# Kernel tuning notes

Hardware: AMD Instinct MI355X
Metric: run time of the kernel (lower is better)

## Reference

```python
import jax, jax.numpy as jnp
import numpy as np

N = 100000
E = 1600000
C = 128
SIM_THRESH = 0.2
DEG_THRESH = 3.0


def setup_inputs() -> dict:
    key = jax.random.key(0)
    ks = jax.random.split(key, 10)
    g = 0.1  # glorot-ish scale for prompt params
    x = jax.random.normal(ks[0], (N, C), jnp.float32)
    edge_index = jax.random.randint(ks[1], (2, E), 0, N)
    prompt_sim = jax.random.normal(ks[2], (1, C), jnp.float32) * g
    prompt_degree = jax.random.normal(ks[3], (1, C), jnp.float32) * g
    prompt_other = jax.random.normal(ks[4], (1, C), jnp.float32) * g
    readout_token = jax.random.normal(ks[5], (1, 1, C), jnp.float32) * g
    in_proj_w = jax.random.normal(ks[6], (3 * C, C), jnp.float32) / np.sqrt(C)
    in_proj_b = jnp.zeros((3 * C,), jnp.float32)
    out_proj_w = jax.random.normal(ks[7], (C, C), jnp.float32) / np.sqrt(C)
    out_proj_b = jnp.zeros((C,), jnp.float32)
    return {"x": x, "prompt_sim": prompt_sim, "prompt_degree": prompt_degree,
            "prompt_other": prompt_other, "readout_token": readout_token,
            "in_proj_w": in_proj_w, "in_proj_b": in_proj_b,
            "out_proj_w": out_proj_w, "out_proj_b": out_proj_b,
            "edge_index": edge_index}


def _forward(x, prompt_sim, prompt_degree, prompt_other, readout_token,
             in_proj_w, in_proj_b, out_proj_w, out_proj_b, edge_index):
    n = x.shape[0]
    row, col = edge_index[0], edge_index[1]

    # per-edge cosine similarity, scatter-added to destination nodes
    x_norm = x / jnp.sqrt(jnp.sum(x * x, axis=1, keepdims=True))  # [N,C]
    e = jnp.sum(x_norm[row] * x_norm[col], axis=1)                # [E]
    c = jax.ops.segment_sum(e, col, num_segments=n)               # [N]
    deg = jax.ops.segment_sum(jnp.ones_like(e), col, num_segments=n)  # [N]
    csim = jax.lax.stop_gradient(c / deg)                         # nan for deg==0 -> mask False

    sim_mask = csim <= SIM_THRESH                                 # [N] bool
    deg_mask = jax.lax.stop_gradient(deg) <= DEG_THRESH
    other_mask = ~(sim_mask | deg_mask)

    neg1 = jnp.float32(-1.0)
    slot0 = jnp.where(sim_mask[:, None], prompt_sim, neg1)        # [N,C]
    slot1 = jnp.where(deg_mask[:, None], prompt_degree, neg1)
    slot2 = jnp.where(other_mask[:, None], prompt_other, neg1)
    rec = jnp.stack([slot0, slot1, slot2], axis=1)                # [N,3,C]
    ro = jnp.broadcast_to(readout_token, (n, 1, x.shape[1]))
    rec = jnp.concatenate([ro, rec], axis=1)                      # [N,4,C]

    # key_padding_mask: True where slot entirely -1 (unfilled)
    kpm = jnp.all(rec == neg1, axis=-1)                           # [N,4]

    # single-head MHA over the 4 prompt slots per node
    qkv = rec @ in_proj_w.T + in_proj_b                           # [N,4,3C]
    q, k, v = jnp.split(qkv, 3, axis=-1)
    scale = 1.0 / np.sqrt(rec.shape[-1])
    scores = jnp.einsum('nqc,nkc->nqk', q, k) * scale             # [N,4,4]
    scores = jnp.where(kpm[:, None, :], -jnp.inf, scores)
    attn = jax.nn.softmax(scores, axis=-1)
    out = jnp.einsum('nqk,nkc->nqc', attn, v)
    out = out @ out_proj_w.T + out_proj_b                         # [N,4,C]

    final = out[:, 0, :]                                          # readout slot
    return x + final


def reference(x, prompt_sim, prompt_degree, prompt_other, readout_token,
              in_proj_w, in_proj_b, out_proj_w, out_proj_b, edge_index):
    return _forward(x, prompt_sim, prompt_degree, prompt_other, readout_token,
                    in_proj_w, in_proj_b, out_proj_w, out_proj_b, edge_index)
```

## Files before the change

### kernel.cpp

```cpp
#include <hip/hip_runtime.h>
#include <hip/hip_bf16.h>
#include <math.h>

#define C 128
#define SIM_THRESH 0.2f
#define DEG_THRESH 3.0f

#define FIX_SCALE 16777216.0f
#define FIX_INV   5.9604644775390625e-8f

typedef float floatx2 __attribute__((ext_vector_type(2)));

__device__ void finals_body(int combo,
                            const float* __restrict__ ps, const float* __restrict__ pd,
                            const float* __restrict__ po, const float* __restrict__ ro,
                            const float* __restrict__ W,  const float* __restrict__ b,
                            const float* __restrict__ Wo, const float* __restrict__ bo,
                            float* __restrict__ finals) {
    bool sim   = (combo & 1) != 0;
    bool degm  = (combo & 2) != 0;
    bool other = !(sim || degm);
    int t = threadIdx.x;

    __shared__ float rec[4][C];
    __shared__ float kk[4][C];
    __shared__ float vv[4][C];
    __shared__ float q0[C];
    __shared__ float out0[C];
    __shared__ float attn[4];

    if (t < C) {
        rec[0][t] = ro[t];
        rec[1][t] = sim   ? ps[t] : -1.0f;
        rec[2][t] = degm  ? pd[t] : -1.0f;
        rec[3][t] = other ? po[t] : -1.0f;
    }
    __syncthreads();

    if (t < C) {
        float accq = b[t];
        for (int i = 0; i < C; ++i) accq += rec[0][i] * W[t * C + i];
        q0[t] = accq;
        for (int j = 0; j < 4; ++j) {
            float ak = b[C + t];
            float av = b[2 * C + t];
            const float* Wk = W + (size_t)(C + t) * C;
            const float* Wv = W + (size_t)(2 * C + t) * C;
            for (int i = 0; i < C; ++i) {
                float r = rec[j][i];
                ak += r * Wk[i];
                av += r * Wv[i];
            }
            kk[j][t] = ak;
            vv[j][t] = av;
        }
    }
    __syncthreads();

    if (t == 0) {
        bool kpm[4] = { false, !sim, !degm, !other };
        const float scale = 0.08838834764831845f;
        float sc[4];
        float m = -INFINITY;
        for (int j = 0; j < 4; ++j) {
            if (kpm[j]) { sc[j] = -INFINITY; continue; }
            float s = 0.0f;
            for (int i = 0; i < C; ++i) s += q0[i] * kk[j][i];
            sc[j] = s * scale;
            m = fmaxf(m, sc[j]);
        }
        float denom = 0.0f;
        for (int j = 0; j < 4; ++j) {
            float e = (sc[j] == -INFINITY) ? 0.0f : expf(sc[j] - m);
            attn[j] = e;
            denom += e;
        }
        for (int j = 0; j < 4; ++j) attn[j] /= denom;
    }
    __syncthreads();

    if (t < C)
        out0[t] = attn[0] * vv[0][t] + attn[1] * vv[1][t] +
                  attn[2] * vv[2][t] + attn[3] * vv[3][t];
    __syncthreads();

    if (t < C) {
        float f = bo[t];
        for (int i = 0; i < C; ++i) f += out0[i] * Wo[t * C + i];
        finals[combo * C + t] = f;
    }
}

__global__ void prep_kernel(const float* __restrict__ x, unsigned int* __restrict__ xn,
                            unsigned long long* __restrict__ packed,
                            const float* __restrict__ ps, const float* __restrict__ pd,
                            const float* __restrict__ po, const float* __restrict__ ro,
                            const float* __restrict__ W,  const float* __restrict__ b,
                            const float* __restrict__ Wo, const float* __restrict__ bo,
                            float* __restrict__ finals, int N, int nRowBlocks) {
    if ((int)blockIdx.x >= nRowBlocks) {
        finals_body(blockIdx.x - nRowBlocks, ps, pd, po, ro, W, b, Wo, bo, finals);
        return;
    }
    int grp = threadIdx.x >> 5;
    int l   = threadIdx.x & 31;
    int row = blockIdx.x * 8 + grp;
    if (row >= N) return;
    float4 a = ((const float4*)(x + (size_t)row * C))[l];
    float s = a.x * a.x + a.y * a.y + a.z * a.z + a.w * a.w;
    #pragma unroll
    for (int off = 16; off; off >>= 1) s += __shfl_xor(s, off, 64);
    float r = rsqrtf(s);
    int u = __builtin_amdgcn_cvt_pk_fp8_f32(a.x * r, a.y * r, 0, false);
    u     = __builtin_amdgcn_cvt_pk_fp8_f32(a.z * r, a.w * r, u, true);
    xn[(size_t)row * 32 + l] = (unsigned int)u;
    if (l == 0) packed[row] = 0ULL;
}

__global__ void edge_kernel_fp8(const uint4* __restrict__ xn4, const int* __restrict__ ei,
                                unsigned long long* __restrict__ packed, int E) {
    int gid  = blockIdx.x * blockDim.x + threadIdx.x;
    int edge = gid >> 3;
    int lane = threadIdx.x & 7;
    if (edge >= E) return;
    int r = ei[edge];
    int c = ei[E + edge];
    uint4 a = xn4[(size_t)r * 8 + lane];
    uint4 b = xn4[(size_t)c * 8 + lane];
    float dot = 0.0f;
    #pragma unroll
    for (int k = 0; k < 4; ++k) {
        int ua = (int)(&a.x)[k], ub = (int)(&b.x)[k];
        floatx2 a0 = __builtin_amdgcn_cvt_pk_f32_fp8(ua, false);
        floatx2 a1 = __builtin_amdgcn_cvt_pk_f32_fp8(ua, true);
        floatx2 b0 = __builtin_amdgcn_cvt_pk_f32_fp8(ub, false);
        floatx2 b1 = __builtin_amdgcn_cvt_pk_f32_fp8(ub, true);
        dot += a0.x * b0.x + a0.y * b0.y + a1.x * b1.x + a1.y * b1.y;
    }
    #pragma unroll
    for (int off = 4; off; off >>= 1) dot += __shfl_xor(dot, off, 64);
    if (lane == 0) {
        long long fx = (long long)llrintf(dot * FIX_SCALE);
        atomicAdd(&packed[c], (1ULL << 40) + (unsigned long long)fx);
    }
}

__global__ void norm_kernel(const float* __restrict__ x, float* __restrict__ rnorm, int N) {
    int row  = (blockIdx.x * blockDim.x + threadIdx.x) >> 6;
    int lane = threadIdx.x & 63;
    if (row >= N) return;
    float2 a = ((const float2*)(x + (size_t)row * C))[lane];
    float s = a.x * a.x + a.y * a.y;
    #pragma unroll
    for (int off = 32; off; off >>= 1) s += __shfl_xor(s, off, 64);
    if (lane == 0) rnorm[row] = rsqrtf(s);
}

__global__ void edge_kernel_f32(const float* __restrict__ x, const int* __restrict__ ei,
                                const float* __restrict__ rnorm,
                                unsigned long long* __restrict__ packed, int E) {
    int edge = (blockIdx.x * blockDim.x + threadIdx.x) >> 5;
    int lane = threadIdx.x & 31;
    if (edge >= E) return;
    int r = ei[edge];
    int c = ei[E + edge];
    float4 a = ((const float4*)(x + (size_t)r * C))[lane];
    float4 b = ((const float4*)(x + (size_t)c * C))[lane];
    float dot = a.x * b.x + a.y * b.y + a.z * b.z + a.w * b.w;
    #pragma unroll
    for (int off = 16; off; off >>= 1) dot += __shfl_xor(dot, off, 64);
    if (lane == 0) {
        float e = dot * rnorm[r] * rnorm[c];
        long long fx = (long long)llrintf(e * FIX_SCALE);
        atomicAdd(&packed[c], (1ULL << 40) + (unsigned long long)fx);
    }
}

__global__ void finals_only_kernel(const float* __restrict__ ps, const float* __restrict__ pd,
                                   const float* __restrict__ po, const float* __restrict__ ro,
                                   const float* __restrict__ W,  const float* __restrict__ b,
                                   const float* __restrict__ Wo, const float* __restrict__ bo,
                                   float* __restrict__ finals) {
    finals_body(blockIdx.x, ps, pd, po, ro, W, b, Wo, bo, finals);
}

__global__ void apply_kernel(const float* __restrict__ x,
                             const unsigned long long* __restrict__ packed,
                             const float* __restrict__ finals,
                             float* __restrict__ out, int N) {
    size_t i = (size_t)blockIdx.x * blockDim.x + threadIdx.x;
    size_t total = (size_t)N * (C / 4);
    if (i >= total) return;
    int row = (int)(i >> 5);
    unsigned long long v = packed[row];
    long long d_ll = (long long)((v + (1ULL << 39)) >> 40);
    long long s_ll = (long long)(v - ((unsigned long long)d_ll << 40));
    float d  = (float)d_ll;
    float cs = (float)s_ll * FIX_INV;
    bool sim  = (d_ll > 0) && ((cs / d) <= SIM_THRESH);
    bool degm = d <= DEG_THRESH;
    int combo = (sim ? 1 : 0) | (degm ? 2 : 0);
    float4 xv = ((const float4*)x)[i];
    float4 fv = ((const float4*)finals)[(size_t)combo * 32 + (i & 31)];
    float4 o  = { xv.x + fv.x, xv.y + fv.y, xv.z + fv.z, xv.w + fv.w };
    ((float4*)out)[i] = o;
}

extern "C" void kernel_launch(void* const* d_in, const int* in_sizes, int n_in,
                              void* d_out, int out_size, void* d_ws, size_t ws_size,
                              hipStream_t stream) {
    const float* x             = (const float*)d_in[0];
    const float* prompt_sim    = (const float*)d_in[1];
    const float* prompt_degree = (const float*)d_in[2];
    const float* prompt_other  = (const float*)d_in[3];
    const float* readout       = (const float*)d_in[4];
    const float* in_proj_w     = (const float*)d_in[5];
    const float* in_proj_b     = (const float*)d_in[6];
    const float* out_proj_w    = (const float*)d_in[7];
    const float* out_proj_b    = (const float*)d_in[8];
    const int*   edge_index    = (const int*)d_in[9];

    const int N = in_sizes[0] / C;
    const int E = in_sizes[9] / 2;
    float* out = (float*)d_out;

    unsigned long long* packed = (unsigned long long*)d_ws;
    float* finals = (float*)(packed + N);
    float* rnorm  = finals + 4 * C;
    size_t head_bytes = ((size_t)N * 8 + (size_t)(4 * C + N) * sizeof(float) + 255) & ~(size_t)255;
    unsigned int* xn = (unsigned int*)((char*)d_ws + head_bytes);
    size_t need = head_bytes + (size_t)N * C;
    bool fp8_path = (ws_size >= need);

    if (fp8_path) {
        int nRowBlocks = (N + 7) / 8;
        prep_kernel<<<nRowBlocks + 4, 256, 0, stream>>>(
            x, xn, packed, prompt_sim, prompt_degree, prompt_other, readout,
            in_proj_w, in_proj_b, out_proj_w, out_proj_b, finals, N, nRowBlocks);
        {
            long long lanes = (long long)E * 8;
            int blocks = (int)((lanes + 255) / 256);
            edge_kernel_fp8<<<blocks, 256, 0, stream>>>((const uint4*)xn, edge_index, packed, E);
        }
    } else {
        hipMemsetAsync(packed, 0, (size_t)N * 8, stream);
        finals_only_kernel<<<4, 256, 0, stream>>>(prompt_sim, prompt_degree, prompt_other,
                                                  readout, in_proj_w, in_proj_b,
                                                  out_proj_w, out_proj_b, finals);
        {
            int blocks = (N * 64 + 255) / 256;
            norm_kernel<<<blocks, 256, 0, stream>>>(x, rnorm, N);
        }
        {
            long long lanes = (long long)E * 32;
            int blocks = (int)((lanes + 255) / 256);
            edge_kernel_f32<<<blocks, 256, 0, stream>>>(x, edge_index, rnorm, packed, E);
        }
    }

    {
        long long work = (long long)N * (C / 4);
        int blocks = (int)((work + 255) / 256);
        apply_kernel<<<blocks, 256, 0, stream>>>(x, packed, finals, out, N);
    }
}
```

Measured before the change: 240.6 us.

## Precompute per-slot q/k/v projections and combine attention finals in edge kernel

Attention for the four mask combos is now factored: q, the four k vectors and the four out-projected v vectors are each computed once by nine parallel wave-reduced GEMV blocks, not recomputed serially per combo by one thread per output. A single extra block in the edge kernel then computes the softmax weights for all combos and mixes the precomputed vectors into the finals. This removes the long serial tail of the old 4-block finals path inside prep, and on the fallback path it replaces the memset with zeroing in the norm kernel. It relies on the -1 slots being masked out, so only the prompt bases matter, and adds one block to the edge launch.

```diff
diff --git a/kernel.cpp b/kernel.cpp
--- a/kernel.cpp
+++ b/kernel.cpp
@@ -11,83 +11,104 @@
 
 typedef float floatx2 __attribute__((ext_vector_type(2)));
 
-__device__ void finals_body(int combo,
-                            const float* __restrict__ ps, const float* __restrict__ pd,
-                            const float* __restrict__ po, const float* __restrict__ ro,
-                            const float* __restrict__ W,  const float* __restrict__ b,
-                            const float* __restrict__ Wo, const float* __restrict__ bo,
-                            float* __restrict__ finals) {
-    bool sim   = (combo & 1) != 0;
-    bool degm  = (combo & 2) != 0;
-    bool other = !(sim || degm);
+__device__ __forceinline__ void gemv_body(int e,
+        const float* __restrict__ ps, const float* __restrict__ pd,
+        const float* __restrict__ po, const float* __restrict__ ro,
+        const float* __restrict__ W,  const float* __restrict__ b,
+        const float* __restrict__ Wo,
+        float* __restrict__ qb, float* __restrict__ kb, float* __restrict__ vpb) {
+    const float* bases[4] = { ro, ps, pd, po };
+    int wave = threadIdx.x >> 6;
+    int lane = threadIdx.x & 63;
+    __shared__ float vbuf[C];
+
+    if (e == 0) {
+        float2 sv = ((const float2*)ro)[lane];
+        for (int t = wave * 32; t < wave * 32 + 32; ++t) {
+            float2 wr = ((const float2*)(W + (size_t)t * C))[lane];
+            float p = wr.x * sv.x + wr.y * sv.y;
+            #pragma unroll
+            for (int off = 32; off; off >>= 1) p += __shfl_xor(p, off, 64);
+            if (lane == 0) qb[t] = p + b[t];
+        }
+    } else if (e <= 4) {
+        int bi = e - 1;
+        float2 sv = ((const float2*)bases[bi])[lane];
+        for (int t = wave * 32; t < wave * 32 + 32; ++t) {
+            float2 wr = ((const float2*)(W + (size_t)(C + t) * C))[lane];
+            float p = wr.x * sv.x + wr.y * sv.y;
+            #pragma unroll
+            for (int off = 32; off; off >>= 1) p += __shfl_xor(p, off, 64);
+            if (lane == 0) kb[bi * C + t] = p + b[C + t];
+        }
+    } else {
+        int bi = e - 5;
+        float2 sv = ((const float2*)bases[bi])[lane];
+        for (int t = wave * 32; t < wave * 32 + 32; ++t) {
+            float2 wr = ((const float2*)(W + (size_t)(2 * C + t) * C))[lane];
+            float p = wr.x * sv.x + wr.y * sv.y;
+            #pragma unroll
+            for (int off = 32; off; off >>= 1) p += __shfl_xor(p, off, 64);
+            if (lane == 0) vbuf[t] = p + b[2 * C + t];
+        }
+        __syncthreads();
+        float2 vv = ((const float2*)vbuf)[lane];
+        for (int t = wave * 32; t < wave * 32 + 32; ++t) {
+            float2 wr = ((const float2*)(Wo + (size_t)t * C))[lane];
+            float p = wr.x * vv.x + wr.y * vv.y;
+            #pragma unroll
+            for (int off = 32; off; off >>= 1) p += __shfl_xor(p, off, 64);
+            if (lane == 0) vpb[bi * C + t] = p;
+        }
+    }
+}
+
+__device__ __forceinline__ void combine_body(
+        const float* __restrict__ qb, const float* __restrict__ kb,
+        const float* __restrict__ vpb, const float* __restrict__ bo,
+        float* __restrict__ finals) {
+    __shared__ float attn_s[4][4];
+    int wv = threadIdx.x >> 6;
+    int lane = threadIdx.x & 63;
+    if (wv == 0) {
+        float2 qv = ((const float2*)qb)[lane];
+        float d[4];
+        #pragma unroll
+        for (int bI = 0; bI < 4; ++bI) {
+            float2 kv = ((const float2*)(kb + bI * C))[lane];
+            float p = qv.x * kv.x + qv.y * kv.y;
+            #pragma unroll
+            for (int off = 32; off; off >>= 1) p += __shfl_xor(p, off, 64);
+            d[bI] = p;
+        }
+        if (lane == 0) {
+            const float scale = 0.08838834764831845f;
+            for (int combo = 0; combo < 4; ++combo) {
+                bool sim = (combo & 1), degm = (combo & 2), other = !(sim || degm);
+                bool act[4] = { true, sim, degm, other };
+                float m = -INFINITY;
+                #pragma unroll
+                for (int j = 0; j < 4; ++j) if (act[j]) m = fmaxf(m, d[j] * scale);
+                float w[4], den = 0.0f;
+                #pragma unroll
+                for (int j = 0; j < 4; ++j) {
+                    w[j] = act[j] ? expf(d[j] * scale - m) : 0.0f;
+                    den += w[j];
+                }
+                #pragma unroll
+                for (int j = 0; j < 4; ++j) attn_s[combo][j] = w[j] / den;
+            }
+        }
+    }
+    __syncthreads();
     int t = threadIdx.x;
-
-    __shared__ float rec[4][C];
-    __shared__ float kk[4][C];
-    __shared__ float vv[4][C];
-    __shared__ float q0[C];
-    __shared__ float out0[C];
-    __shared__ float attn[4];
-
     if (t < C) {
-        rec[0][t] = ro[t];
-        rec[1][t] = sim   ? ps[t] : -1.0f;
-        rec[2][t] = degm  ? pd[t] : -1.0f;
-        rec[3][t] = other ? po[t] : -1.0f;
-    }
-    __syncthreads();
-
-    if (t < C) {
-        float accq = b[t];
-        for (int i = 0; i < C; ++i) accq += rec[0][i] * W[t * C + i];
-        q0[t] = accq;
-        for (int j = 0; j < 4; ++j) {
-            float ak = b[C + t];
-            float av = b[2 * C + t];
-            const float* Wk = W + (size_t)(C + t) * C;
-            const float* Wv = W + (size_t)(2 * C + t) * C;
-            for (int i = 0; i < C; ++i) {
-                float r = rec[j][i];
-                ak += r * Wk[i];
-                av += r * Wv[i];
-            }
-            kk[j][t] = ak;
-            vv[j][t] = av;
-        }
-    }
-    __syncthreads();
-
-    if (t == 0) {
-        bool kpm[4] = { false, !sim, !degm, !other };
-        const float scale = 0.08838834764831845f;
-        float sc[4];
-        float m = -INFINITY;
-        for (int j = 0; j < 4; ++j) {
-            if (kpm[j]) { sc[j] = -INFINITY; continue; }
-            float s = 0.0f;
-            for (int i = 0; i < C; ++i) s += q0[i] * kk[j][i];
-            sc[j] = s * scale;
-            m = fmaxf(m, sc[j]);
-        }
-        float denom = 0.0f;
-        for (int j = 0; j < 4; ++j) {
-            float e = (sc[j] == -INFINITY) ? 0.0f : expf(sc[j] - m);
-            attn[j] = e;
-            denom += e;
-        }
-        for (int j = 0; j < 4; ++j) attn[j] /= denom;
-    }
-    __syncthreads();
-
-    if (t < C)
-        out0[t] = attn[0] * vv[0][t] + attn[1] * vv[1][t] +
-                  attn[2] * vv[2][t] + attn[3] * vv[3][t];
-    __syncthreads();
-
-    if (t < C) {
-        float f = bo[t];
-        for (int i = 0; i < C; ++i) f += out0[i] * Wo[t * C + i];
-        finals[combo * C + t] = f;
+        for (int combo = 0; combo < 4; ++combo) {
+            float f = bo[t];
+            #pragma unroll
+            for (int j = 0; j < 4; ++j) f += attn_s[combo][j] * vpb[j * C + t];
+            finals[combo * C + t] = f;
+        }
     }
 }
 
@@ -96,15 +117,16 @@
                             const float* __restrict__ ps, const float* __restrict__ pd,
                             const float* __restrict__ po, const float* __restrict__ ro,
                             const float* __restrict__ W,  const float* __restrict__ b,
-                            const float* __restrict__ Wo, const float* __restrict__ bo,
-                            float* __restrict__ finals, int N, int nRowBlocks) {
-    if ((int)blockIdx.x >= nRowBlocks) {
-        finals_body(blockIdx.x - nRowBlocks, ps, pd, po, ro, W, b, Wo, bo, finals);
+                            const float* __restrict__ Wo,
+                            float* __restrict__ qb, float* __restrict__ kb,
+                            float* __restrict__ vpb, int N) {
+    if (blockIdx.x < 9) {
+        gemv_body(blockIdx.x, ps, pd, po, ro, W, b, Wo, qb, kb, vpb);
         return;
     }
     int grp = threadIdx.x >> 5;
     int l   = threadIdx.x & 31;
-    int row = blockIdx.x * 8 + grp;
+    int row = (blockIdx.x - 9) * 8 + grp;
     if (row >= N) return;
     float4 a = ((const float4*)(x + (size_t)row * C))[l];
     float s = a.x * a.x + a.y * a.y + a.z * a.z + a.w * a.w;
@@ -118,8 +140,15 @@
 }
 
 __global__ void edge_kernel_fp8(const uint4* __restrict__ xn4, const int* __restrict__ ei,
-                                unsigned long long* __restrict__ packed, int E) {
-    int gid  = blockIdx.x * blockDim.x + threadIdx.x;
+                                unsigned long long* __restrict__ packed, int E,
+                                const float* __restrict__ qb, const float* __restrict__ kb,
+                                const float* __restrict__ vpb, const float* __restrict__ bo,
+                                float* __restrict__ finals) {
+    if (blockIdx.x == 0) {
+        combine_body(qb, kb, vpb, bo, finals);
+        return;
+    }
+    int gid  = (blockIdx.x - 1) * blockDim.x + threadIdx.x;
     int edge = gid >> 3;
     int lane = threadIdx.x & 7;
     if (edge >= E) return;
@@ -145,7 +174,17 @@
     }
 }
 
-__global__ void norm_kernel(const float* __restrict__ x, float* __restrict__ rnorm, int N) {
+__global__ void gemv_kernel(const float* __restrict__ ps, const float* __restrict__ pd,
+                            const float* __restrict__ po, const float* __restrict__ ro,
+                            const float* __restrict__ W,  const float* __restrict__ b,
+                            const float* __restrict__ Wo,
+                            float* __restrict__ qb, float* __restrict__ kb,
+                            float* __restrict__ vpb) {
+    gemv_body(blockIdx.x, ps, pd, po, ro, W, b, Wo, qb, kb, vpb);
+}
+
+__global__ void norm_kernel(const float* __restrict__ x, float* __restrict__ rnorm,
+                            unsigned long long* __restrict__ packed, int N) {
     int row  = (blockIdx.x * blockDim.x + threadIdx.x) >> 6;
     int lane = threadIdx.x & 63;
     if (row >= N) return;
@@ -153,13 +192,21 @@
     float s = a.x * a.x + a.y * a.y;
     #pragma unroll
     for (int off = 32; off; off >>= 1) s += __shfl_xor(s, off, 64);
-    if (lane == 0) rnorm[row] = rsqrtf(s);
+    if (lane == 0) { rnorm[row] = rsqrtf(s); packed[row] = 0ULL; }
 }
 
 __global__ void edge_kernel_f32(const float* __restrict__ x, const int* __restrict__ ei,
                                 const float* __restrict__ rnorm,
-                                unsigned long long* __restrict__ packed, int E) {
-    int edge = (blockIdx.x * blockDim.x + threadIdx.x) >> 5;
+                                unsigned long long* __restrict__ packed, int E,
+                                const float* __restrict__ qb, const float* __restrict__ kb,
+                                const float* __restrict__ vpb, const float* __restrict__ bo,
+                                float* __restrict__ finals) {
+    if (blockIdx.x == 0) {
+        combine_body(qb, kb, vpb, bo, finals);
+        return;
+    }
+    int gid  = (blockIdx.x - 1) * blockDim.x + threadIdx.x;
+    int edge = gid >> 5;
     int lane = threadIdx.x & 31;
     if (edge >= E) return;
     int r = ei[edge];
@@ -174,14 +221,6 @@
         long long fx = (long long)llrintf(e * FIX_SCALE);
         atomicAdd(&packed[c], (1ULL << 40) + (unsigned long long)fx);
     }
-}
-
-__global__ void finals_only_kernel(const float* __restrict__ ps, const float* __restrict__ pd,
-                                   const float* __restrict__ po, const float* __restrict__ ro,
-                                   const float* __restrict__ W,  const float* __restrict__ b,
-                                   const float* __restrict__ Wo, const float* __restrict__ bo,
-                                   float* __restrict__ finals) {
-    finals_body(blockIdx.x, ps, pd, po, ro, W, b, Wo, bo, finals);
 }
 
 __global__ void apply_kernel(const float* __restrict__ x,
@@ -226,35 +265,38 @@
 
     unsigned long long* packed = (unsigned long long*)d_ws;
     float* finals = (float*)(packed + N);
-    float* rnorm  = finals + 4 * C;
-    size_t head_bytes = ((size_t)N * 8 + (size_t)(4 * C + N) * sizeof(float) + 255) & ~(size_t)255;
+    float* qb     = finals + 4 * C;
+    float* kb     = qb + C;
+    float* vpb    = kb + 4 * C;
+    float* rnorm  = vpb + 4 * C;
+    size_t head_bytes = ((size_t)N * 8 + (size_t)(13 * C + N) * sizeof(float) + 255) & ~(size_t)255;
     unsigned int* xn = (unsigned int*)((char*)d_ws + head_bytes);
     size_t need = head_bytes + (size_t)N * C;
     bool fp8_path = (ws_size >= need);
 
     if (fp8_path) {
         int nRowBlocks = (N + 7) / 8;
-        prep_kernel<<<nRowBlocks + 4, 256, 0, stream>>>(
+        prep_kernel<<<nRowBlocks + 9, 256, 0, stream>>>(
             x, xn, packed, prompt_sim, prompt_degree, prompt_other, readout,
-            in_proj_w, in_proj_b, out_proj_w, out_proj_b, finals, N, nRowBlocks);
+            in_proj_w, in_proj_b, out_proj_w, qb, kb, vpb, N);
         {
             long long lanes = (long long)E * 8;
-            int blocks = (int)((lanes + 255) / 256);
-            edge_kernel_fp8<<<blocks, 256, 0, stream>>>((const uint4*)xn, edge_index, packed, E);
+            int blocks = 1 + (int)((lanes + 255) / 256);
+            edge_kernel_fp8<<<blocks, 256, 0, stream>>>((const uint4*)xn, edge_index, packed, E,
+                                                        qb, kb, vpb, out_proj_b, finals);
         }
     } else {
-        hipMemsetAsync(packed, 0, (size_t)N * 8, stream);
-        finals_only_kernel<<<4, 256, 0, stream>>>(prompt_sim, prompt_degree, prompt_other,
-                                                  readout, in_proj_w, in_proj_b,
-                                                  out_proj_w, out_proj_b, finals);
+        gemv_kernel<<<9, 256, 0, stream>>>(prompt_sim, prompt_degree, prompt_other, readout,
+                                           in_proj_w, in_proj_b, out_proj_w, qb, kb, vpb);
         {
             int blocks = (N * 64 + 255) / 256;
-            norm_kernel<<<blocks, 256, 0, stream>>>(x, rnorm, N);
+            norm_kernel<<<blocks, 256, 0, stream>>>(x, rnorm, packed, N);
         }
         {
             long long lanes = (long long)E * 32;
-            int blocks = (int)((lanes + 255) / 256);
-            edge_kernel_f32<<<blocks, 256, 0, stream>>>(x, edge_index, rnorm, packed, E);
+            int blocks = 1 + (int)((lanes + 255) / 256);
+            edge_kernel_f32<<<blocks, 256, 0, stream>>>(x, edge_index, rnorm, packed, E,
+                                                        qb, kb, vpb, out_proj_b, finals);
         }
     }
 
```

Result: faster. 233.9 us (-2.8%).
